# Kernel tuning notes

Measured on AMD Instinct MI355X. Metric: run time of the kernel, lower is better.

Reference implementation:

```python
import jax, jax.numpy as jnp
import numpy as np

D_MODEL = 1024

def setup_inputs() -> dict:
    key = jax.random.key(0)
    kx, kq, kk, kv, ko = jax.random.split(key, 5)
    B, S, D = 8, 2048, D_MODEL
    scale = 1.0 / np.sqrt(D)
    x = jax.random.normal(kx, (B, S, D), dtype=jnp.float32)
    # nn.Linear weights are [out, in]; y = x @ W.T
    Wq = jax.random.normal(kq, (D, D), dtype=jnp.float32) * scale
    Wk = jax.random.normal(kk, (D, D), dtype=jnp.float32) * scale
    Wv = jax.random.normal(kv, (D, D), dtype=jnp.float32) * scale
    Wo = jax.random.normal(ko, (D, D), dtype=jnp.float32) * scale
    return {"x": x, "Wq": Wq, "Wk": Wk, "Wv": Wv, "Wo": Wo}

def reference(x, Wq, Wk, Wv, Wo):
    # Single-head self-attention, dropout in eval mode (identity).
    d_model = x.shape[-1]
    q = jnp.einsum('bsd,ed->bse', x, Wq)
    k = jnp.einsum('bsd,ed->bse', x, Wk)
    v = jnp.einsum('bsd,ed->bse', x, Wv)
    scores = jnp.einsum('bqe,bke->bqk', q, k) / jnp.sqrt(jnp.float32(d_model))
    attn = jax.nn.softmax(scores, axis=-1)
    weighted = jnp.einsum('bqk,bke->bqe', attn, v)
    return jnp.einsum('bqe,oe->bqo', weighted, Wo)
```

## Files before the change

kernel.cpp:

```cpp
#include <hip/hip_runtime.h>
#include <hip/hip_bf16.h>
#include <stdint.h>

typedef short bf16x8 __attribute__((ext_vector_type(8)));
typedef float f32x4 __attribute__((ext_vector_type(4)));

__device__ __forceinline__ unsigned short f2bf(float x) {
  uint32_t u = __builtin_bit_cast(uint32_t, x);
  u += 0x7FFFu + ((u >> 16) & 1u);
  return (unsigned short)(u >> 16);
}
__device__ __forceinline__ float bf2f(unsigned short u) {
  uint32_t v = ((uint32_t)u) << 16;
  return __builtin_bit_cast(float, v);
}

__device__ __forceinline__ void gl2lds16(const void* g, void* l) {
  __builtin_amdgcn_global_load_lds(
      (const __attribute__((address_space(1))) unsigned int*)g,
      (__attribute__((address_space(3))) unsigned int*)l, 16, 0, 0);
}

__global__ __launch_bounds__(256) void cast_f32_bf16_k(
    const float* __restrict__ s, unsigned short* __restrict__ d, long n) {
  long i = ((long)blockIdx.x * 256 + threadIdx.x) * 8;
  if (i >= n) return;
  float4 a = *(const float4*)(s + i);
  float4 b = *(const float4*)(s + i + 4);
  bf16x8 o;
  o[0] = (short)f2bf(a.x); o[1] = (short)f2bf(a.y);
  o[2] = (short)f2bf(a.z); o[3] = (short)f2bf(a.w);
  o[4] = (short)f2bf(b.x); o[5] = (short)f2bf(b.y);
  o[6] = (short)f2bf(b.z); o[7] = (short)f2bf(b.w);
  *(bf16x8*)(d + i) = o;
}

__global__ __launch_bounds__(256) void cast4_f32_bf16_k(
    const float* __restrict__ s0, const float* __restrict__ s1,
    const float* __restrict__ s2, const float* __restrict__ s3,
    unsigned short* __restrict__ d, long n) {
  const float* s = blockIdx.z == 0 ? s0 : blockIdx.z == 1 ? s1 : blockIdx.z == 2 ? s2 : s3;
  long i = ((long)blockIdx.x * 256 + threadIdx.x) * 8;
  if (i >= n) return;
  float4 a = *(const float4*)(s + i);
  float4 b = *(const float4*)(s + i + 4);
  bf16x8 o;
  o[0] = (short)f2bf(a.x); o[1] = (short)f2bf(a.y);
  o[2] = (short)f2bf(a.z); o[3] = (short)f2bf(a.w);
  o[4] = (short)f2bf(b.x); o[5] = (short)f2bf(b.y);
  o[6] = (short)f2bf(b.z); o[7] = (short)f2bf(b.w);
  *(bf16x8*)(d + blockIdx.z * n + i) = o;
}

template <typename OutT>
__global__ __launch_bounds__(512, 2) void gemm_tt(
    const unsigned short* __restrict__ A, const unsigned short* __restrict__ B,
    OutT* __restrict__ C, int K,
    long sA, long sB, long sC, int ldA, int ldB, int ldT, float alpha) {
  extern __shared__ __align__(16) char smem[];
  const int bz = blockIdx.z;
  const int gx = gridDim.x;
  const int nwg = gx * gridDim.y;
  const int idx = blockIdx.y * gx + blockIdx.x;
  const int wg = (idx & 7) * (nwg >> 3) + (idx >> 3);
  const int bm = wg / gx, bn = wg % gx;

  const int tid = threadIdx.x, lane = tid & 63, wave = tid >> 6;
  const int wm = wave >> 2, wn = wave & 3;

  const long ldAb = (long)ldA * 2, ldBb = (long)ldB * 2;
  const char* Ac = (const char*)(A + (long)bz * sA) + (long)bm * 256 * ldAb;
  const char* Bc = (const char*)(B + (long)bz * sB) + (long)bn * 256 * ldBb;
  C += (long)bz * sC;

  const int sr8 = tid >> 3;
  const int scolx = (((tid & 7) ^ ((tid >> 3) & 7)) << 4);

  auto stageHalf = [&](int t, int op, int h, const char* gbase, long ldb_) {
    char* reg = smem + (((((t & 1) << 1) | op) << 1 | h) << 14);
    const long ktb = (long)t << 7;
#pragma unroll
    for (int c = 0; c < 2; ++c)
      gl2lds16(gbase + (long)(h * 128 + c * 64 + sr8) * ldb_ + ktb + scolx,
               reg + c * 8192 + tid * 16);
  };

  const char* Areg[2] = { smem + ((0 << 2 | wm) << 14),
                          smem + ((1 << 2 | wm) << 14) };
  const char* Breg[2] = { smem + (((0 << 2) | 2 | (wn >> 1)) << 14),
                          smem + (((1 << 2) | 2 | (wn >> 1)) << 14) };
  const int cko[2] = { (((lane >> 4) << 4) ^ ((lane & 7) << 4)),
                       ((64 | ((lane >> 4) << 4)) ^ ((lane & 7) << 4)) };
  const int rowA0 = (lane & 15) * 128;
  const int rowB0 = ((wn & 1) * 64 + (lane & 15)) * 128;

  f32x4 acc[8][4] = {};

  stageHalf(0, 1, 0, Bc, ldBb); stageHalf(0, 1, 1, Bc, ldBb);
  stageHalf(0, 0, 0, Ac, ldAb); stageHalf(0, 0, 1, Ac, ldAb);
  stageHalf(1, 1, 0, Bc, ldBb); stageHalf(1, 1, 1, Bc, ldBb);
  asm volatile("s_waitcnt vmcnt(4)" ::: "memory");
  __builtin_amdgcn_s_barrier();

  const int nt = K >> 6;
  const int niter = nt >> 1;
  for (int i = 0; i < niter; ++i) {
    const int u = 2 * i;
    const bool pf = (i + 1 < niter);
#pragma unroll
    for (int d = 0; d < 2; ++d) {
      bf16x8 b[4][2];
#pragma unroll
      for (int mq = 0; mq < 4; ++mq) {
        bf16x8 a[2][2];
        if (mq == 0) {
#pragma unroll
          for (int n = 0; n < 4; ++n)
#pragma unroll
            for (int kh = 0; kh < 2; ++kh)
              b[n][kh] = *(const bf16x8*)(Breg[d] + rowB0 + n * 2048 + cko[kh]);
        }
#pragma unroll
        for (int j = 0; j < 2; ++j)
#pragma unroll
          for (int kh = 0; kh < 2; ++kh)
            a[j][kh] = *(const bf16x8*)(Areg[d] + rowA0 + (mq * 2 + j) * 2048 + cko[kh]);
        if (d == 0 && mq == 0) { stageHalf(u + 1, 0, 0, Ac, ldAb); stageHalf(u + 1, 0, 1, Ac, ldAb); }
        if (d == 0 && mq == 1 && pf) stageHalf(u + 2, 1, 0, Bc, ldBb);
        if (d == 0 && mq == 2 && pf) stageHalf(u + 2, 1, 1, Bc, ldBb);
        if (d == 1 && mq == 0 && pf) { stageHalf(u + 2, 0, 0, Ac, ldAb); stageHalf(u + 2, 0, 1, Ac, ldAb); }
        if (d == 1 && mq == 1 && pf) stageHalf(u + 3, 1, 0, Bc, ldBb);
        if (d == 1 && mq == 2 && pf) stageHalf(u + 3, 1, 1, Bc, ldBb);
        if (mq == 0) asm volatile("s_waitcnt lgkmcnt(8)" ::: "memory");
        __builtin_amdgcn_s_barrier();
        asm volatile("s_waitcnt lgkmcnt(0)" ::: "memory");
        __builtin_amdgcn_sched_barrier(0);
        __builtin_amdgcn_s_setprio(1);
#pragma unroll
        for (int kh = 0; kh < 2; ++kh)
#pragma unroll
          for (int j = 0; j < 2; ++j)
#pragma unroll
            for (int n = 0; n < 4; ++n)
              acc[mq * 2 + j][n] = __builtin_amdgcn_mfma_f32_16x16x32_bf16(
                  a[j][kh], b[n][kh], acc[mq * 2 + j][n], 0, 0, 0);
        __builtin_amdgcn_s_setprio(0);
        if (d == 0 && mq == 3) {
          if (pf) asm volatile("s_waitcnt vmcnt(4)" ::: "memory");
          else    asm volatile("s_waitcnt vmcnt(0)" ::: "memory");
        }
        if (d == 1 && mq == 3 && pf) asm volatile("s_waitcnt vmcnt(4)" ::: "memory");
        __builtin_amdgcn_s_barrier();
      }
    }
  }

  const long row0 = (long)bm * 256 + wm * 128 + (lane >> 4) * 4;
  const int col0 = bn * 256 + wn * 64 + (lane & 15);
#pragma unroll
  for (int m = 0; m < 8; ++m) {
#pragma unroll
    for (int n = 0; n < 4; ++n) {
      long row = row0 + m * 16;
      long col = col0 + n * 16;
      long base = col * (long)ldT + row;
      if constexpr (sizeof(OutT) == 2) {
        ushort4 st;
        st.x = f2bf(acc[m][n][0] * alpha); st.y = f2bf(acc[m][n][1] * alpha);
        st.z = f2bf(acc[m][n][2] * alpha); st.w = f2bf(acc[m][n][3] * alpha);
        *(ushort4*)((unsigned short*)C + base) = st;
      } else {
        float4 st;
        st.x = acc[m][n][0] * alpha; st.y = acc[m][n][1] * alpha;
        st.z = acc[m][n][2] * alpha; st.w = acc[m][n][3] * alpha;
        *(float4*)((float*)C + base) = st;
      }
    }
  }
}

__global__ __launch_bounds__(256) void softmax_inplace(unsigned short* __restrict__ s, int C) {
  __shared__ float red[8];
  long row = blockIdx.x;
  unsigned short* p = s + row * (long)C;
  int tid = threadIdx.x, lane = tid & 63, w = tid >> 6;
  bf16x8 raw = *(const bf16x8*)(p + tid * 8);
  float v[8];
  float mx = -3.4e38f;
#pragma unroll
  for (int j = 0; j < 8; ++j) { v[j] = bf2f((unsigned short)raw[j]); mx = fmaxf(mx, v[j]); }
#pragma unroll
  for (int o = 32; o > 0; o >>= 1) mx = fmaxf(mx, __shfl_xor(mx, o));
  if (lane == 0) red[w] = mx;
  __syncthreads();
  mx = fmaxf(fmaxf(red[0], red[1]), fmaxf(red[2], red[3]));
  float sum = 0.f;
#pragma unroll
  for (int j = 0; j < 8; ++j) { v[j] = __expf(v[j] - mx); sum += v[j]; }
#pragma unroll
  for (int o = 32; o > 0; o >>= 1) sum += __shfl_xor(sum, o);
  if (lane == 0) red[4 + w] = sum;
  __syncthreads();
  float inv = 1.f / (red[4] + red[5] + red[6] + red[7]);
  bf16x8 o8;
#pragma unroll
  for (int j = 0; j < 8; ++j) o8[j] = (short)f2bf(v[j] * inv);
  *(bf16x8*)(p + tid * 8) = o8;
}

extern "C" void kernel_launch(void* const* d_in, const int* in_sizes, int n_in,
                              void* d_out, int out_size, void* d_ws, size_t ws_size,
                              hipStream_t stream) {
  (void)in_sizes; (void)n_in; (void)out_size; (void)ws_size;
  const float* x  = (const float*)d_in[0];
  const float* Wq = (const float*)d_in[1];
  const float* Wk = (const float*)d_in[2];
  const float* Wv = (const float*)d_in[3];
  const float* Wo = (const float*)d_in[4];
  const int B = 8, S = 2048, D = 1024;
  const long MB = 1 << 20;
  char* w = (char*)d_ws;
  unsigned short* Wqb = (unsigned short*)(w + 0 * MB);
  unsigned short* Wkb = (unsigned short*)(w + 2 * MB);
  unsigned short* Wvb = (unsigned short*)(w + 4 * MB);
  unsigned short* Wob = (unsigned short*)(w + 6 * MB);
  unsigned short* xb  = (unsigned short*)(w + 8 * MB);
  unsigned short* qb  = (unsigned short*)(w + 40 * MB);
  unsigned short* kb  = (unsigned short*)(w + 72 * MB);
  unsigned short* vt  = (unsigned short*)(w + 104 * MB);
  unsigned short* wb  = xb;
  unsigned short* attn = (unsigned short*)d_out;
  float* out = (float*)d_out;

  long nx = (long)B * S * D;
  long nw = (long)D * D;

  const int LDSB = 131072;
  hipFuncSetAttribute((const void*)gemm_tt<unsigned short>,
                      hipFuncAttributeMaxDynamicSharedMemorySize, LDSB);
  hipFuncSetAttribute((const void*)gemm_tt<float>,
                      hipFuncAttributeMaxDynamicSharedMemorySize, LDSB);

  cast_f32_bf16_k<<<(int)(nx / 2048), 256, 0, stream>>>(x, xb, nx);
  dim3 gW((int)(nw / 2048), 1, 4);
  cast4_f32_bf16_k<<<gW, 256, 0, stream>>>(Wq, Wk, Wv, Wo, Wqb, nw);

  dim3 gQ(64, 4, 1);
  gemm_tt<unsigned short><<<gQ, 512, LDSB, stream>>>(
      Wqb, xb, qb, D, 0, 0, 0, D, D, D, 1.f);
  gemm_tt<unsigned short><<<gQ, 512, LDSB, stream>>>(
      Wkb, xb, kb, D, 0, 0, 0, D, D, D, 1.f);
  dim3 gV(4, 64, 1);
  gemm_tt<unsigned short><<<gV, 512, LDSB, stream>>>(
      xb, Wvb, vt, D, 0, 0, 0, D, D, B * S, 1.f);

  dim3 gS(8, 8, B);
  gemm_tt<unsigned short><<<gS, 512, LDSB, stream>>>(
      kb, qb, attn, D, (long)S * D, (long)S * D, (long)S * S, D, D, S, 0.03125f);

  softmax_inplace<<<B * S, 256, 0, stream>>>(attn, S);

  dim3 gPV(8, 4, B);
  gemm_tt<unsigned short><<<gPV, 512, LDSB, stream>>>(
      vt, attn, wb, S, (long)S, (long)S * S, (long)S * D, B * S, S, D, 1.f);

  dim3 gO(64, 4, 1);
  gemm_tt<float><<<gO, 512, LDSB, stream>>>(
      Wob, wb, out, D, 0, 0, 0, D, D, D, 1.f);
}
```

Measured before the change: 343.8 us.

## Double-buffer A fragment LDS reads across MFMA groups in GEMM inner loop

Restructures the GEMM main loop so each k-half loads one B fragment set and ping-pongs two A register buffers. The next A fragment's LDS read is issued before the current MFMA block runs, hiding LDS latency behind matrix math. It also halves live B/A fragment registers per step. In exchange it adds more barriers, since there are now eight sub-steps per d instead of four, and relies on hand-tuned lgkmcnt counts whose correctness around the interleaved global-to-LDS stages is delicate.

```diff
diff --git a/kernel.cpp b/kernel.cpp
--- a/kernel.cpp
+++ b/kernel.cpp
@@ -109,48 +109,66 @@
     const bool pf = (i + 1 < niter);
 #pragma unroll
     for (int d = 0; d < 2; ++d) {
-      bf16x8 b[4][2];
-#pragma unroll
-      for (int mq = 0; mq < 4; ++mq) {
-        bf16x8 a[2][2];
-        if (mq == 0) {
-#pragma unroll
-          for (int n = 0; n < 4; ++n)
-#pragma unroll
-            for (int kh = 0; kh < 2; ++kh)
-              b[n][kh] = *(const bf16x8*)(Breg[d] + rowB0 + n * 2048 + cko[kh]);
+      bf16x8 b[4], a0[2], a1[2];
+#pragma unroll
+      for (int n = 0; n < 4; ++n)
+        b[n] = *(const bf16x8*)(Breg[d] + rowB0 + n * 2048 + cko[0]);
+#pragma unroll
+      for (int j = 0; j < 2; ++j)
+        a0[j] = *(const bf16x8*)(Areg[d] + rowA0 + j * 2048 + cko[0]);
+#pragma unroll
+      for (int kh = 0; kh < 2; ++kh) {
+#pragma unroll
+        for (int mq = 0; mq < 4; ++mq) {
+          if (kh == 0 && mq == 0) {
+            if (d == 0) { stageHalf(u+1,0,0,Ac,ldAb); stageHalf(u+1,0,1,Ac,ldAb); }
+            else if (pf) { stageHalf(u+2,0,0,Ac,ldAb); stageHalf(u+2,0,1,Ac,ldAb); }
+          }
+          if (kh == 1 && pf) {
+            if (d == 0 && mq == 1) stageHalf(u+2,1,0,Bc,ldBb);
+            if (d == 0 && mq == 2) stageHalf(u+2,1,1,Bc,ldBb);
+            if (d == 1 && mq == 1) stageHalf(u+3,1,0,Bc,ldBb);
+            if (d == 1 && mq == 2) stageHalf(u+3,1,1,Bc,ldBb);
+          }
+          bf16x8* cur = (mq & 1) ? a1 : a0;
+          bf16x8* nxt = (mq & 1) ? a0 : a1;
+          if (mq < 3) {
+#pragma unroll
+            for (int j = 0; j < 2; ++j)
+              nxt[j] = *(const bf16x8*)(Areg[d] + rowA0 + ((mq+1)*2 + j) * 2048 + cko[kh]);
+            asm volatile("s_waitcnt lgkmcnt(2)" ::: "memory");
+          } else if (kh == 0) {
+#pragma unroll
+            for (int j = 0; j < 2; ++j)
+              nxt[j] = *(const bf16x8*)(Areg[d] + rowA0 + j * 2048 + cko[1]);
+            asm volatile("s_waitcnt lgkmcnt(2)" ::: "memory");
+          } else {
+            asm volatile("s_waitcnt lgkmcnt(0)" ::: "memory");
+          }
+          __builtin_amdgcn_sched_barrier(0);
+          __builtin_amdgcn_s_setprio(1);
+#pragma unroll
+          for (int j = 0; j < 2; ++j)
+#pragma unroll
+            for (int n = 0; n < 4; ++n)
+              acc[mq*2+j][n] = __builtin_amdgcn_mfma_f32_16x16x32_bf16(
+                  cur[j], b[n], acc[mq*2+j][n], 0, 0, 0);
+          __builtin_amdgcn_s_setprio(0);
+          if (kh == 0 && mq == 3) {
+#pragma unroll
+            for (int n = 0; n < 4; ++n)
+              b[n] = *(const bf16x8*)(Breg[d] + rowB0 + n * 2048 + cko[1]);
+          }
+          if (kh == 1 && mq == 3) {
+            if (d == 0) {
+              if (pf) asm volatile("s_waitcnt vmcnt(4)" ::: "memory");
+              else    asm volatile("s_waitcnt vmcnt(0)" ::: "memory");
+            } else if (pf) {
+              asm volatile("s_waitcnt vmcnt(4)" ::: "memory");
+            }
+          }
+          __builtin_amdgcn_s_barrier();
         }
-#pragma unroll
-        for (int j = 0; j < 2; ++j)
-#pragma unroll
-          for (int kh = 0; kh < 2; ++kh)
-            a[j][kh] = *(const bf16x8*)(Areg[d] + rowA0 + (mq * 2 + j) * 2048 + cko[kh]);
-        if (d == 0 && mq == 0) { stageHalf(u + 1, 0, 0, Ac, ldAb); stageHalf(u + 1, 0, 1, Ac, ldAb); }
-        if (d == 0 && mq == 1 && pf) stageHalf(u + 2, 1, 0, Bc, ldBb);
-        if (d == 0 && mq == 2 && pf) stageHalf(u + 2, 1, 1, Bc, ldBb);
-        if (d == 1 && mq == 0 && pf) { stageHalf(u + 2, 0, 0, Ac, ldAb); stageHalf(u + 2, 0, 1, Ac, ldAb); }
-        if (d == 1 && mq == 1 && pf) stageHalf(u + 3, 1, 0, Bc, ldBb);
-        if (d == 1 && mq == 2 && pf) stageHalf(u + 3, 1, 1, Bc, ldBb);
-        if (mq == 0) asm volatile("s_waitcnt lgkmcnt(8)" ::: "memory");
-        __builtin_amdgcn_s_barrier();
-        asm volatile("s_waitcnt lgkmcnt(0)" ::: "memory");
-        __builtin_amdgcn_sched_barrier(0);
-        __builtin_amdgcn_s_setprio(1);
-#pragma unroll
-        for (int kh = 0; kh < 2; ++kh)
-#pragma unroll
-          for (int j = 0; j < 2; ++j)
-#pragma unroll
-            for (int n = 0; n < 4; ++n)
-              acc[mq * 2 + j][n] = __builtin_amdgcn_mfma_f32_16x16x32_bf16(
-                  a[j][kh], b[n][kh], acc[mq * 2 + j][n], 0, 0, 0);
-        __builtin_amdgcn_s_setprio(0);
-        if (d == 0 && mq == 3) {
-          if (pf) asm volatile("s_waitcnt vmcnt(4)" ::: "memory");
-          else    asm volatile("s_waitcnt vmcnt(0)" ::: "memory");
-        }
-        if (d == 1 && mq == 3 && pf) asm volatile("s_waitcnt vmcnt(4)" ::: "memory");
-        __builtin_amdgcn_s_barrier();
       }
     }
   }
```

Measured after the change: 341.5 us. No clear change (-0.7%).

## Software-pipeline LDS fragment loads with register double-buffering in GEMM loop

Applied to the files above, without the earlier changes.

The GEMM main loop now keeps double-buffered register fragments for A and B. The next quarter's A fragments, and at stage boundaries the next stage's B fragments, are read from LDS while the current MFMAs run. This replaces the old per-quarter pattern of load, barrier, wait for lgkmcnt(0), then compute, which exposed LDS latency before each MFMA batch. It costs more VGPRs for the extra fragment buffers and relies on hand-tuned waitcnt counts and barrier placement, so register pressure or a sync error could hurt occupancy or correctness.

```diff
diff --git a/kernel.cpp b/kernel.cpp
--- a/kernel.cpp
+++ b/kernel.cpp
@@ -95,12 +95,23 @@
   const int rowB0 = ((wn & 1) * 64 + (lane & 15)) * 128;
 
   f32x4 acc[8][4] = {};
+  bf16x8 b2[2][4][2], a0[2][2], a1[2][2];
 
   stageHalf(0, 1, 0, Bc, ldBb); stageHalf(0, 1, 1, Bc, ldBb);
   stageHalf(0, 0, 0, Ac, ldAb); stageHalf(0, 0, 1, Ac, ldAb);
   stageHalf(1, 1, 0, Bc, ldBb); stageHalf(1, 1, 1, Bc, ldBb);
   asm volatile("s_waitcnt vmcnt(4)" ::: "memory");
   __builtin_amdgcn_s_barrier();
+#pragma unroll
+  for (int n = 0; n < 4; ++n)
+#pragma unroll
+    for (int kh = 0; kh < 2; ++kh)
+      b2[0][n][kh] = *(const bf16x8*)(Breg[0] + rowB0 + n * 2048 + cko[kh]);
+#pragma unroll
+  for (int j = 0; j < 2; ++j)
+#pragma unroll
+    for (int kh = 0; kh < 2; ++kh)
+      a0[j][kh] = *(const bf16x8*)(Areg[0] + rowA0 + j * 2048 + cko[kh]);
 
   const int nt = K >> 6;
   const int niter = nt >> 1;
@@ -109,31 +120,45 @@
     const bool pf = (i + 1 < niter);
 #pragma unroll
     for (int d = 0; d < 2; ++d) {
-      bf16x8 b[4][2];
 #pragma unroll
       for (int mq = 0; mq < 4; ++mq) {
-        bf16x8 a[2][2];
         if (mq == 0) {
-#pragma unroll
-          for (int n = 0; n < 4; ++n)
+          if (d == 0) { stageHalf(u+1,0,0,Ac,ldAb); stageHalf(u+1,0,1,Ac,ldAb); }
+          else if (pf) { stageHalf(u+2,0,0,Ac,ldAb); stageHalf(u+2,0,1,Ac,ldAb); }
+        }
+        if (mq == 1 && pf) stageHalf(u+2+d,1,0,Bc,ldBb);
+        if (mq == 2 && pf) stageHalf(u+2+d,1,1,Bc,ldBb);
+
+        bf16x8 (*cur)[2] = (mq & 1) ? a1 : a0;
+        bf16x8 (*nxt)[2] = (mq & 1) ? a0 : a1;
+        if (mq < 3) {
+#pragma unroll
+          for (int j = 0; j < 2; ++j)
 #pragma unroll
             for (int kh = 0; kh < 2; ++kh)
-              b[n][kh] = *(const bf16x8*)(Breg[d] + rowB0 + n * 2048 + cko[kh]);
+              nxt[j][kh] = *(const bf16x8*)(Areg[d] + rowA0 + ((mq+1)*2 + j) * 2048 + cko[kh]);
+          asm volatile("s_waitcnt lgkmcnt(4)" ::: "memory");
+        } else {
+          const bool haveNext = (d == 0) || pf;
+          if (haveNext) {
+            if (d == 0 && !pf) asm volatile("s_waitcnt vmcnt(0)" ::: "memory");
+            else               asm volatile("s_waitcnt vmcnt(4)" ::: "memory");
+            __builtin_amdgcn_s_barrier();
+#pragma unroll
+            for (int n = 0; n < 4; ++n)
+#pragma unroll
+              for (int kh = 0; kh < 2; ++kh)
+                b2[d^1][n][kh] = *(const bf16x8*)(Breg[d^1] + rowB0 + n * 2048 + cko[kh]);
+#pragma unroll
+            for (int j = 0; j < 2; ++j)
+#pragma unroll
+              for (int kh = 0; kh < 2; ++kh)
+                nxt[j][kh] = *(const bf16x8*)(Areg[d^1] + rowA0 + j * 2048 + cko[kh]);
+            asm volatile("s_waitcnt lgkmcnt(12)" ::: "memory");
+          } else {
+            asm volatile("s_waitcnt lgkmcnt(0)" ::: "memory");
+          }
         }
-#pragma unroll
-        for (int j = 0; j < 2; ++j)
-#pragma unroll
-          for (int kh = 0; kh < 2; ++kh)
-            a[j][kh] = *(const bf16x8*)(Areg[d] + rowA0 + (mq * 2 + j) * 2048 + cko[kh]);
-        if (d == 0 && mq == 0) { stageHalf(u + 1, 0, 0, Ac, ldAb); stageHalf(u + 1, 0, 1, Ac, ldAb); }
-        if (d == 0 && mq == 1 && pf) stageHalf(u + 2, 1, 0, Bc, ldBb);
-        if (d == 0 && mq == 2 && pf) stageHalf(u + 2, 1, 1, Bc, ldBb);
-        if (d == 1 && mq == 0 && pf) { stageHalf(u + 2, 0, 0, Ac, ldAb); stageHalf(u + 2, 0, 1, Ac, ldAb); }
-        if (d == 1 && mq == 1 && pf) stageHalf(u + 3, 1, 0, Bc, ldBb);
-        if (d == 1 && mq == 2 && pf) stageHalf(u + 3, 1, 1, Bc, ldBb);
-        if (mq == 0) asm volatile("s_waitcnt lgkmcnt(8)" ::: "memory");
-        __builtin_amdgcn_s_barrier();
-        asm volatile("s_waitcnt lgkmcnt(0)" ::: "memory");
         __builtin_amdgcn_sched_barrier(0);
         __builtin_amdgcn_s_setprio(1);
 #pragma unroll
@@ -142,14 +167,9 @@
           for (int j = 0; j < 2; ++j)
 #pragma unroll
             for (int n = 0; n < 4; ++n)
-              acc[mq * 2 + j][n] = __builtin_amdgcn_mfma_f32_16x16x32_bf16(
-                  a[j][kh], b[n][kh], acc[mq * 2 + j][n], 0, 0, 0);
+              acc[mq*2+j][n] = __builtin_amdgcn_mfma_f32_16x16x32_bf16(
+                  cur[j][kh], b2[d][n][kh], acc[mq*2+j][n], 0, 0, 0);
         __builtin_amdgcn_s_setprio(0);
-        if (d == 0 && mq == 3) {
-          if (pf) asm volatile("s_waitcnt vmcnt(4)" ::: "memory");
-          else    asm volatile("s_waitcnt vmcnt(0)" ::: "memory");
-        }
-        if (d == 1 && mq == 3 && pf) asm volatile("s_waitcnt vmcnt(4)" ::: "memory");
         __builtin_amdgcn_s_barrier();
       }
     }
```

Result: slower. 641.5 us (+86.6%).
